# Kernel optimization log

Hardware: AMD Instinct MI355X
Metric: run time of the kernel (lower is better)

## Reference

```python
import jax, jax.numpy as jnp
import numpy as np

N_SCALES = 3
BASE_SIGMA = 0.1
SCALES = jnp.asarray([BASE_SIGMA * 2.0 ** i for i in range(N_SCALES)], dtype=jnp.float32)


def setup_inputs() -> dict:
    key = jax.random.key(0)
    k_x, k_pos, k_tp, k_w1, k_b1, k_w2, k_b2 = jax.random.split(key, 7)
    B, C, T = 16, 306, 4000
    M = 128
    x = jax.random.normal(k_x, (B, C, T), dtype=jnp.float32)
    positions = jax.random.normal(k_pos, (B, C, 2), dtype=jnp.float32)
    target_positions = jax.random.normal(k_tp, (M, 2), dtype=jnp.float32)
    # nn.Linear(3, 32) / nn.Linear(32, 1) params (kaiming-uniform-ish init)
    lim1 = 1.0 / np.sqrt(3.0)
    w1 = jax.random.uniform(k_w1, (3, 32), jnp.float32, -lim1, lim1)
    b1 = jax.random.uniform(k_b1, (32,), jnp.float32, -lim1, lim1)
    lim2 = 1.0 / np.sqrt(32.0)
    w2 = jax.random.uniform(k_w2, (32, 1), jnp.float32, -lim2, lim2)
    b2 = jax.random.uniform(k_b2, (1,), jnp.float32, -lim2, lim2)
    return {"x": x, "positions": positions, "target_positions": target_positions,
            "w1": w1, "b1": b1, "w2": w2, "b2": b2}


def reference(x, positions, target_positions, w1, b1, w2, b2):
    # squared euclidean distances [B, C, M]
    diff = positions[:, :, None, :] - target_positions[None, None, :, :]
    d2 = jnp.sum(diff * diff, axis=-1)
    # multi-scale Gaussian kernels, stacked on last axis -> [B, C, M, n_scales]
    inv = 1.0 / (2.0 * SCALES ** 2)  # [n_scales]
    scale_weights = jnp.exp(-d2[..., None] * inv)
    # tiny 2-layer MLP gate: (3 -> 32 -> 1)
    h = jax.nn.relu(scale_weights @ w1 + b1)  # [B, C, M, 32]
    w = (h @ w2 + b2)[..., 0]                 # [B, C, M]
    # normalize over channel dim
    w = w / (jnp.sum(w, axis=1, keepdims=True) + 1e-8)
    # weighted channel aggregation -> [B, M, T]
    return jnp.einsum('bct,bcm->bmt', x, w)
```

## Files before the change

kernel.cpp:

```cpp
#include <hip/hip_runtime.h>

#define B_ 16
#define C_ 306
#define T_ 4000
#define M_ 128

typedef short bf16x8 __attribute__((ext_vector_type(8)));
typedef float f32x4 __attribute__((ext_vector_type(4)));

#define WF_PER_B 81920

__global__ __launch_bounds__(320)
void gate_kernel(const float* __restrict__ positions,
                 const float* __restrict__ target,
                 const float* __restrict__ w1,
                 const float* __restrict__ b1,
                 const float* __restrict__ w2,
                 const float* __restrict__ b2,
                 unsigned short* __restrict__ wf,
                 float* __restrict__ scale) {
    const int b  = blockIdx.x >> 5;
    const int mg = blockIdx.x & 31;
    const int tid = threadIdx.x;

    __shared__ float s_w1[96], s_b1[32], s_w2[32];
    __shared__ float s_b2;
    __shared__ float s_tgt[8];
    __shared__ float s_part[4][5];
    __shared__ unsigned short s_frag[40 * 72];

    if (tid < 96) s_w1[tid] = w1[tid];
    if (tid < 32) { s_b1[tid] = b1[tid]; s_w2[tid] = w2[tid]; }
    if (tid == 256) s_b2 = b2[0];
    if (tid >= 312) s_tgt[tid - 312] = target[mg * 8 + (tid - 312)];
    __syncthreads();

    float px = 0.0f, py = 0.0f;
    if (tid < C_) {
        px = positions[(b * C_ + tid) * 2 + 0];
        py = positions[(b * C_ + tid) * 2 + 1];
    }

    float wv_[4];
#pragma unroll
    for (int mi = 0; mi < 4; ++mi) {
        float w = 0.0f;
        if (tid < C_) {
            const float dx = px - s_tgt[mi * 2 + 0];
            const float dy = py - s_tgt[mi * 2 + 1];
            const float d2 = dx * dx + dy * dy;
            const float s2 = __expf(-d2 * 3.125f);
            const float q  = s2 * s2;
            const float s1 = q * q;
            const float r  = s1 * s1;
            const float s0 = r * r;
            float acc = s_b2;
#pragma unroll
            for (int j = 0; j < 32; ++j) {
                float h = fmaf(s0, s_w1[j],
                          fmaf(s1, s_w1[32 + j],
                          fmaf(s2, s_w1[64 + j], s_b1[j])));
                acc = fmaf(fmaxf(h, 0.0f), s_w2[j], acc);
            }
            w = acc;
        }
        wv_[mi] = w;
    }

#pragma unroll
    for (int mi = 0; mi < 4; ++mi) {
        float s = wv_[mi];
#pragma unroll
        for (int off = 32; off > 0; off >>= 1) s += __shfl_down(s, off, 64);
        if ((tid & 63) == 0) s_part[mi][tid >> 6] = s;
    }

    const int chunk = tid >> 3;
    const int slot  = tid & 7;
#pragma unroll
    for (int mi = 0; mi < 4; ++mi) {
        const float w = wv_[mi];
        const unsigned int u = __float_as_uint(w);
        const unsigned short h = (unsigned short)(u >> 16);
        const float lof = w - __uint_as_float(u & 0xffff0000u);
        const unsigned short l = (unsigned short)(__float_as_uint(lof) >> 16);
        s_frag[chunk * 72 + mi * 16 + 0 + slot] = h;
        s_frag[chunk * 72 + mi * 16 + 8 + slot] = l;
    }
    __syncthreads();

    if (tid < 4) {
        float tot = s_part[tid][0] + s_part[tid][1] + s_part[tid][2]
                  + s_part[tid][3] + s_part[tid][4];
        scale[b * M_ + mg * 4 + tid] = 1.0f / (tot + 1e-8f);
    }

    {
        const int ch = tid >> 3;
        const int g  = tid & 7;
        const uint4 v = *(const uint4*)(s_frag + ch * 72 + g * 8);
        unsigned short* dst = wf + (size_t)b * WF_PER_B
                            + (size_t)ch * 2048 + mg * 64 + g * 8;
        *(uint4*)dst = v;
    }
}

#define RS3 160

__global__ __launch_bounds__(256, 2)
void merge_gemm(const float* __restrict__ x,
                const unsigned short* __restrict__ wf,
                const float* __restrict__ scale,
                float* __restrict__ out) {
    const int t0 = blockIdx.x * 64;
    const int b  = blockIdx.y;
    const int tid  = threadIdx.x;
    const int lane = tid & 63;
    const int wv   = tid >> 6;
    const int tquad = lane >> 4;
    const int tsub  = lane & 15;

    __shared__ __align__(16) unsigned int sX[2][64 * RS3];

    const float* xb = x + (size_t)b * C_ * T_;
    const unsigned short* wfB = wf + (size_t)b * WF_PER_B;

    const int cp = tid >> 4;
    const int TQ = tid & 15;
    const float* xcol = xb + min(t0 + TQ * 4, T_ - 4);

#pragma unroll
    for (int half = 0; half < 2; ++half) {
        float4 va[5], vb[5];
#pragma unroll
        for (int j = 0; j < 5; ++j) {
            const int k = half * 5 + j;
            const int c = k * 32 + 2 * cp;
            va[j] = *(const float4*)(xcol + (size_t)min(c,     C_ - 1) * T_);
            vb[j] = *(const float4*)(xcol + (size_t)min(c + 1, C_ - 1) * T_);
        }
#pragma unroll
        for (int j = 0; j < 5; ++j) {
            const int k = half * 5 + j;
            const int p = k * 16 + cp;
            const float* fa = (const float*)&va[j];
            const float* fb = (const float*)&vb[j];
#pragma unroll
            for (int tt = 0; tt < 4; ++tt) {
                const int t = TQ * 4 + tt;
                const int addr = t * RS3 + (p ^ ((t & 7) << 2));
                const unsigned int ua = __float_as_uint(fa[tt]);
                const unsigned int ub = __float_as_uint(fb[tt]);
                const float la = fa[tt] - __uint_as_float(ua & 0xffff0000u);
                const float lb = fb[tt] - __uint_as_float(ub & 0xffff0000u);
                sX[0][addr] = __builtin_amdgcn_perm(ub, ua, 0x07060302u);
                sX[1][addr] = __builtin_amdgcn_perm(__float_as_uint(lb),
                                                    __float_as_uint(la),
                                                    0x07060302u);
            }
        }
    }
    asm volatile("s_waitcnt lgkmcnt(0)" ::: "memory");
    __builtin_amdgcn_s_barrier();
    asm volatile("" ::: "memory");

    f32x4 acc[4][2];
#pragma unroll
    for (int i = 0; i < 4; ++i)
#pragma unroll
        for (int j = 0; j < 2; ++j) acc[i][j] = (f32x4){0.f, 0.f, 0.f, 0.f};

    const int mw  = (wv & 1) * 64;
    const int tw2 = (wv >> 1) * 32;

    auto loadW = [&](int k, bf16x8* ah_, bf16x8* al_) {
#pragma unroll
        for (int mi = 0; mi < 4; ++mi) {
            const size_t aoff = ((size_t)(k * 4 + tquad) * 128
                               + (mw + mi * 16 + tsub)) * 16;
            ah_[mi] = *(const bf16x8*)(wfB + aoff);
            al_[mi] = *(const bf16x8*)(wfB + aoff + 8);
        }
    };

    int rbase[2], tswz[2];
#pragma unroll
    for (int ti = 0; ti < 2; ++ti) {
        const int t = tw2 + ti * 16 + tsub;
        rbase[ti] = t * RS3;
        tswz[ti]  = (t & 7) << 2;
    }

    bf16x8 ah[4], al[4];
    loadW(0, ah, al);

#pragma unroll
    for (int k = 0; k < 10; ++k) {
        bf16x8 bh[2], bl[2];
#pragma unroll
        for (int ti = 0; ti < 2; ++ti) {
            const int q = rbase[ti] + ((k * 16 + tquad * 4) ^ tswz[ti]);
            bh[ti] = *(const bf16x8*)(&sX[0][q]);
            bl[ti] = *(const bf16x8*)(&sX[1][q]);
        }

#pragma unroll
        for (int mi = 0; mi < 4; ++mi)
#pragma unroll
            for (int ti = 0; ti < 2; ++ti)
                acc[mi][ti] = __builtin_amdgcn_mfma_f32_16x16x32_bf16(
                    ah[mi], bh[ti], acc[mi][ti], 0, 0, 0);
#pragma unroll
        for (int mi = 0; mi < 4; ++mi)
#pragma unroll
            for (int ti = 0; ti < 2; ++ti)
                acc[mi][ti] = __builtin_amdgcn_mfma_f32_16x16x32_bf16(
                    ah[mi], bl[ti], acc[mi][ti], 0, 0, 0);
#pragma unroll
        for (int mi = 0; mi < 4; ++mi)
#pragma unroll
            for (int ti = 0; ti < 2; ++ti)
                acc[mi][ti] = __builtin_amdgcn_mfma_f32_16x16x32_bf16(
                    al[mi], bh[ti], acc[mi][ti], 0, 0, 0);

        if (k < 9) loadW(k + 1, ah, al);
    }

#pragma unroll
    for (int mi = 0; mi < 4; ++mi) {
        const int mbase = mw + mi * 16 + tquad * 4;
        const float4 sc = *(const float4*)(scale + b * M_ + mbase);
        float* op = out + ((size_t)b * M_ + mbase) * T_;
#pragma unroll
        for (int ti = 0; ti < 2; ++ti) {
            const int tg = t0 + tw2 + ti * 16 + tsub;
            if (tg < T_) {
                op[(size_t)0 * T_ + tg] = acc[mi][ti][0] * sc.x;
                op[(size_t)1 * T_ + tg] = acc[mi][ti][1] * sc.y;
                op[(size_t)2 * T_ + tg] = acc[mi][ti][2] * sc.z;
                op[(size_t)3 * T_ + tg] = acc[mi][ti][3] * sc.w;
            }
        }
    }
}

extern "C" void kernel_launch(void* const* d_in, const int* in_sizes, int n_in,
                              void* d_out, int out_size, void* d_ws, size_t ws_size,
                              hipStream_t stream) {
    const float* x         = (const float*)d_in[0];
    const float* positions = (const float*)d_in[1];
    const float* target    = (const float*)d_in[2];
    const float* w1        = (const float*)d_in[3];
    const float* b1        = (const float*)d_in[4];
    const float* w2        = (const float*)d_in[5];
    const float* b2        = (const float*)d_in[6];
    float* out = (float*)d_out;

    float* scale = (float*)d_ws;
    unsigned short* wf = (unsigned short*)(scale + B_ * M_);

    gate_kernel<<<B_ * 32, 320, 0, stream>>>(positions, target, w1, b1, w2, b2,
                                             wf, scale);

    dim3 grid((T_ + 63) / 64, B_);
    merge_gemm<<<grid, 256, 0, stream>>>(x, wf, scale, out);
}
```

Baseline: 153.5 us.

## Use 512-thread blocks with smaller per-wave tiles and interleaved LDS hi/lo layout

Doubles merge_gemm block size to 512 threads (8 waves), so each wave computes a 32x32 output tile instead of 64x32, halving accumulators and weight fragments per wave. The x tile is staged in a single pass, with hi and lo bf16 halves interleaved in one row-strided shared array. The first weight fragment load is issued before the LDS stores so it overlaps them. This targets more waves in flight and better latency hiding, at the cost of each wave reusing weight fragments less and more redundant weight loads per block.

```diff
diff --git a/kernel.cpp b/kernel.cpp
--- a/kernel.cpp
+++ b/kernel.cpp
@@ -105,9 +105,9 @@
     }
 }
 
-#define RS3 160
-
-__global__ __launch_bounds__(256, 2)
+#define RS4 320
+
+__global__ __launch_bounds__(512, 4)
 void merge_gemm(const float* __restrict__ x,
                 const unsigned short* __restrict__ wf,
                 const float* __restrict__ scale,
@@ -120,62 +120,17 @@
     const int tquad = lane >> 4;
     const int tsub  = lane & 15;
 
-    __shared__ __align__(16) unsigned int sX[2][64 * RS3];
+    __shared__ __align__(16) unsigned int sX[64 * RS4];
 
     const float* xb = x + (size_t)b * C_ * T_;
     const unsigned short* wfB = wf + (size_t)b * WF_PER_B;
 
-    const int cp = tid >> 4;
-    const int TQ = tid & 15;
-    const float* xcol = xb + min(t0 + TQ * 4, T_ - 4);
-
-#pragma unroll
-    for (int half = 0; half < 2; ++half) {
-        float4 va[5], vb[5];
-#pragma unroll
-        for (int j = 0; j < 5; ++j) {
-            const int k = half * 5 + j;
-            const int c = k * 32 + 2 * cp;
-            va[j] = *(const float4*)(xcol + (size_t)min(c,     C_ - 1) * T_);
-            vb[j] = *(const float4*)(xcol + (size_t)min(c + 1, C_ - 1) * T_);
-        }
-#pragma unroll
-        for (int j = 0; j < 5; ++j) {
-            const int k = half * 5 + j;
-            const int p = k * 16 + cp;
-            const float* fa = (const float*)&va[j];
-            const float* fb = (const float*)&vb[j];
-#pragma unroll
-            for (int tt = 0; tt < 4; ++tt) {
-                const int t = TQ * 4 + tt;
-                const int addr = t * RS3 + (p ^ ((t & 7) << 2));
-                const unsigned int ua = __float_as_uint(fa[tt]);
-                const unsigned int ub = __float_as_uint(fb[tt]);
-                const float la = fa[tt] - __uint_as_float(ua & 0xffff0000u);
-                const float lb = fb[tt] - __uint_as_float(ub & 0xffff0000u);
-                sX[0][addr] = __builtin_amdgcn_perm(ub, ua, 0x07060302u);
-                sX[1][addr] = __builtin_amdgcn_perm(__float_as_uint(lb),
-                                                    __float_as_uint(la),
-                                                    0x07060302u);
-            }
-        }
-    }
-    asm volatile("s_waitcnt lgkmcnt(0)" ::: "memory");
-    __builtin_amdgcn_s_barrier();
-    asm volatile("" ::: "memory");
-
-    f32x4 acc[4][2];
-#pragma unroll
-    for (int i = 0; i < 4; ++i)
-#pragma unroll
-        for (int j = 0; j < 2; ++j) acc[i][j] = (f32x4){0.f, 0.f, 0.f, 0.f};
-
-    const int mw  = (wv & 1) * 64;
-    const int tw2 = (wv >> 1) * 32;
+    const int mw  = (wv & 3) * 32;
+    const int tw2 = (wv >> 2) * 32;
 
     auto loadW = [&](int k, bf16x8* ah_, bf16x8* al_) {
 #pragma unroll
-        for (int mi = 0; mi < 4; ++mi) {
+        for (int mi = 0; mi < 2; ++mi) {
             const size_t aoff = ((size_t)(k * 4 + tquad) * 128
                                + (mw + mi * 16 + tsub)) * 16;
             ah_[mi] = *(const bf16x8*)(wfB + aoff);
@@ -183,16 +138,55 @@
         }
     };
 
+    const int cp = tid & 31;
+    const int TQ = tid >> 5;
+    const float* xcol = xb + min(t0 + TQ * 4, T_ - 4);
+
+    bf16x8 ah[2], al[2];
+
+    float4 va[5], vb[5];
+#pragma unroll
+    for (int j = 0; j < 5; ++j) {
+        const int c = (j * 32 + cp) * 2;
+        va[j] = *(const float4*)(xcol + (size_t)min(c,     C_ - 1) * T_);
+        vb[j] = *(const float4*)(xcol + (size_t)min(c + 1, C_ - 1) * T_);
+    }
+    loadW(0, ah, al);
+
+#pragma unroll
+    for (int j = 0; j < 5; ++j) {
+        const int p = j * 32 + cp;
+        const float* fa = (const float*)&va[j];
+        const float* fb = (const float*)&vb[j];
+#pragma unroll
+        for (int tt = 0; tt < 4; ++tt) {
+            const int t = TQ * 4 + tt;
+            const int q = t * RS4 + (p ^ ((t & 7) << 2));
+            const unsigned int ua = __float_as_uint(fa[tt]);
+            const unsigned int ub = __float_as_uint(fb[tt]);
+            const float la = fa[tt] - __uint_as_float(ua & 0xffff0000u);
+            const float lb = fb[tt] - __uint_as_float(ub & 0xffff0000u);
+            sX[q]       = __builtin_amdgcn_perm(ub, ua, 0x07060302u);
+            sX[q + 160] = __builtin_amdgcn_perm(__float_as_uint(lb),
+                                                __float_as_uint(la),
+                                                0x07060302u);
+        }
+    }
+    __syncthreads();
+
+    f32x4 acc[2][2];
+#pragma unroll
+    for (int i = 0; i < 2; ++i)
+#pragma unroll
+        for (int j = 0; j < 2; ++j) acc[i][j] = (f32x4){0.f, 0.f, 0.f, 0.f};
+
     int rbase[2], tswz[2];
 #pragma unroll
     for (int ti = 0; ti < 2; ++ti) {
         const int t = tw2 + ti * 16 + tsub;
-        rbase[ti] = t * RS3;
+        rbase[ti] = t * RS4;
         tswz[ti]  = (t & 7) << 2;
     }
-
-    bf16x8 ah[4], al[4];
-    loadW(0, ah, al);
 
 #pragma unroll
     for (int k = 0; k < 10; ++k) {
@@ -200,24 +194,24 @@
 #pragma unroll
         for (int ti = 0; ti < 2; ++ti) {
             const int q = rbase[ti] + ((k * 16 + tquad * 4) ^ tswz[ti]);
-            bh[ti] = *(const bf16x8*)(&sX[0][q]);
-            bl[ti] = *(const bf16x8*)(&sX[1][q]);
-        }
-
-#pragma unroll
-        for (int mi = 0; mi < 4; ++mi)
+            bh[ti] = *(const bf16x8*)(&sX[q]);
+            bl[ti] = *(const bf16x8*)(&sX[q + 160]);
+        }
+
+#pragma unroll
+        for (int mi = 0; mi < 2; ++mi)
 #pragma unroll
             for (int ti = 0; ti < 2; ++ti)
                 acc[mi][ti] = __builtin_amdgcn_mfma_f32_16x16x32_bf16(
                     ah[mi], bh[ti], acc[mi][ti], 0, 0, 0);
 #pragma unroll
-        for (int mi = 0; mi < 4; ++mi)
+        for (int mi = 0; mi < 2; ++mi)
 #pragma unroll
             for (int ti = 0; ti < 2; ++ti)
                 acc[mi][ti] = __builtin_amdgcn_mfma_f32_16x16x32_bf16(
                     ah[mi], bl[ti], acc[mi][ti], 0, 0, 0);
 #pragma unroll
-        for (int mi = 0; mi < 4; ++mi)
+        for (int mi = 0; mi < 2; ++mi)
 #pragma unroll
             for (int ti = 0; ti < 2; ++ti)
                 acc[mi][ti] = __builtin_amdgcn_mfma_f32_16x16x32_bf16(
@@ -227,7 +221,7 @@
     }
 
 #pragma unroll
-    for (int mi = 0; mi < 4; ++mi) {
+    for (int mi = 0; mi < 2; ++mi) {
         const int mbase = mw + mi * 16 + tquad * 4;
         const float4 sc = *(const float4*)(scale + b * M_ + mbase);
         float* op = out + ((size_t)b * M_ + mbase) * T_;
@@ -263,5 +257,5 @@
                                              wf, scale);
 
     dim3 grid((T_ + 63) / 64, B_);
-    merge_gemm<<<grid, 256, 0, stream>>>(x, wf, scale, out);
+    merge_gemm<<<grid, 512, 0, stream>>>(x, wf, scale, out);
 }
```

Measured after the change: 156.3 us. No clear change (+1.8%).
